# Performance work log

Measured on AMD Instinct MI355X. Metric: run time of the kernel, lower is better.

## Reference

```python
import jax, jax.numpy as jnp
import numpy as np

B, L, J, D_MODEL, N_HIDDEN = 8, 2048, 2048, 1024, 1024


def setup_inputs() -> dict:
    key = jax.random.key(0)
    ks = jax.random.split(key, 6)
    scale = 1.0 / np.sqrt(D_MODEL)
    return {
        "q": jax.random.normal(ks[0], (B, L, D_MODEL), dtype=jnp.float32),
        "k": jax.random.normal(ks[1], (B, J, D_MODEL), dtype=jnp.float32),
        "v": jax.random.normal(ks[2], (B, J, D_MODEL), dtype=jnp.float32),
        "mask": jnp.zeros((B, L, J), dtype=jnp.float32),
        # Linear(d_model, n_hidden, bias=False) weights, stored [n_hidden, d_model] like torch
        "W_q": jax.random.normal(ks[3], (N_HIDDEN, D_MODEL), dtype=jnp.float32) * scale,
        "W_k": jax.random.normal(ks[4], (N_HIDDEN, D_MODEL), dtype=jnp.float32) * scale,
        "W_v": jax.random.normal(ks[5], (N_HIDDEN, D_MODEL), dtype=jnp.float32) * scale,
    }


def reference(q, k, v, mask, W_q, W_k, W_v):
    # Linear projections (torch Linear: x @ W.T)
    qp = jnp.einsum('bld,hd->blh', q, W_q)
    kp = jnp.einsum('bjd,hd->bjh', k, W_k)
    vp = jnp.einsum('bjd,hd->bjh', v, W_v)
    # scaled dot-product scores [B, L, J]
    scores = jnp.einsum('blh,bjh->blj', qp, kp) / jnp.sqrt(jnp.float32(N_HIDDEN)).astype(qp.dtype)
    scores = scores + mask
    attn = jax.nn.softmax(scores, axis=-1)
    return jnp.einsum('blj,bjh->blh', attn, vp)
```

## Files before the change

kernel.cpp:

```cpp
#include <hip/hip_runtime.h>
#include <hip/hip_fp16.h>

typedef _Float16 f16;
typedef __attribute__((ext_vector_type(8))) _Float16 f16x8;
typedef __attribute__((ext_vector_type(4))) _Float16 f16x4;
typedef __attribute__((ext_vector_type(4))) float f32x4;

#define BM 128
#define BN 128
#define BK 64

__device__ __forceinline__ void gll16(const void* src, void* dst) {
  __builtin_amdgcn_global_load_lds((const __attribute__((address_space(1))) void*)src,
                                   (__attribute__((address_space(3))) void*)dst,
                                   16, 0, 0);
}

template<int MODE>
__global__ __launch_bounds__(256, 3)
void gemm_bt(const f16* __restrict__ Aall, const f16* __restrict__ Ball,
             void* __restrict__ Call,
             int M, int N, int K, int lda, int ldb, int ldc,
             long strideA, long strideB, long strideC,
             const float* __restrict__ maskAll, long strideMask,
             float* __restrict__ lvec, float scale)
{
  __shared__ __align__(16) f16 smA[BM * BK];
  __shared__ __align__(16) f16 smB[BN * BK];

  unsigned gx = gridDim.x, gy = gridDim.y;
  unsigned id = (blockIdx.z * gy + blockIdx.y) * gx + blockIdx.x;
  unsigned nwg = gx * gy * gridDim.z;
  unsigned swz = (id & 7) * (nwg >> 3) + (id >> 3);
  unsigned bx = swz % gx, rem = swz / gx;
  unsigned by = rem % gy, bz = rem / gy;

  const int z = bz;
  const f16* A = Aall + (long)z * strideA;
  const f16* B = Ball + (long)z * strideB;

  const int tid  = threadIdx.x;
  const int wid  = tid >> 6;
  const int lane = tid & 63;
  const int wm = wid >> 1;
  const int wn = wid & 1;
  const int lr = lane & 15;
  const int g  = lane >> 4;

  const long brow = (long)by * BM;
  const long bcol = (long)bx * BN;
  const int  nt   = K / BK;

  f32x4 acc[4][4] = {};

  auto stA = [&](int t) {
    #pragma unroll
    for (int i = 0; i < 4; ++i) {
      int c  = i * 256 + tid;
      int r  = c >> 3;
      int sl = (c & 7) ^ (r & 7);
      gll16(A + (brow + r) * (long)lda + t * BK + sl * 8, &smA[c * 8]);
    }
  };
  auto stB = [&](int t) {
    #pragma unroll
    for (int i = 0; i < 4; ++i) {
      int c  = i * 256 + tid;
      int r  = c >> 3;
      int sl = (c & 7) ^ (r & 7);
      gll16(B + (bcol + r) * (long)ldb + t * BK + sl * 8, &smB[c * 8]);
    }
  };

  for (int t = 0; t < nt; ++t) {
    stA(t); stB(t);
    __syncthreads();
    f16x8 af[8], bf[8];
    #pragma unroll
    for (int fm = 0; fm < 4; ++fm)
      #pragma unroll
      for (int ks = 0; ks < 2; ++ks) {
        int r = wm * 64 + fm * 16 + lr;
        af[fm * 2 + ks] = *(const f16x8*)(smA + r * BK + ((ks * 4 + g) ^ (r & 7)) * 8);
      }
    #pragma unroll
    for (int fn = 0; fn < 4; ++fn)
      #pragma unroll
      for (int ks = 0; ks < 2; ++ks) {
        int r = wn * 64 + fn * 16 + lr;
        bf[fn * 2 + ks] = *(const f16x8*)(smB + r * BK + ((ks * 4 + g) ^ (r & 7)) * 8);
      }
    #pragma unroll
    for (int fm = 0; fm < 4; ++fm)
      #pragma unroll
      for (int fn = 0; fn < 4; ++fn)
        #pragma unroll
        for (int ks = 0; ks < 2; ++ks)
          acc[fm][fn] = __builtin_amdgcn_mfma_f32_16x16x32_f16(
              af[fm * 2 + ks], bf[fn * 2 + ks], acc[fm][fn], 0, 0, 0);
    __syncthreads();
  }

  const int rb = (lane >> 4) * 4;

  if (MODE == 0) {
    f16* C = (f16*)Call + (long)z * strideC;
    #pragma unroll
    for (int m = 0; m < 4; ++m)
      #pragma unroll
      for (int j = 0; j < 4; ++j) {
        long grow = brow + wm * 64 + m * 16 + rb + j;
        #pragma unroll
        for (int n = 0; n < 4; ++n) {
          long gcol = bcol + wn * 64 + n * 16 + lr;
          C[grow * ldc + gcol] = (f16)acc[m][n][j];
        }
      }
  } else if (MODE == 1) {
    f16* C = (f16*)Call + (long)z * strideC;
    const float* mask = maskAll + (long)z * strideMask;
    #pragma unroll
    for (int m = 0; m < 4; ++m)
      #pragma unroll
      for (int j = 0; j < 4; ++j) {
        long grow = brow + wm * 64 + m * 16 + rb + j;
        float s = 0.f;
        #pragma unroll
        for (int n = 0; n < 4; ++n) {
          long gcol = bcol + wn * 64 + n * 16 + lr;
          float p = __expf(acc[m][n][j] * scale + mask[grow * ldc + gcol]);
          C[grow * ldc + gcol] = (f16)p;
          s += p;
        }
        s += __shfl_xor(s, 1);
        s += __shfl_xor(s, 2);
        s += __shfl_xor(s, 4);
        s += __shfl_xor(s, 8);
        if (lr == 0)
          lvec[((long)z * M + grow) * 32 + bx * 2 + wn] = s;
      }
  } else {
    float* C = (float*)Call + (long)z * strideC;
    #pragma unroll
    for (int m = 0; m < 4; ++m)
      #pragma unroll
      for (int j = 0; j < 4; ++j) {
        long grow = brow + wm * 64 + m * 16 + rb + j;
        float inv = 1.0f / lvec[(long)z * M + grow];
        #pragma unroll
        for (int n = 0; n < 4; ++n) {
          long gcol = bcol + wn * 64 + n * 16 + lr;
          C[grow * ldc + gcol] = acc[m][n][j] * inv;
        }
      }
  }
}

__global__ void cvt_all(const float* __restrict__ q, const float* __restrict__ k,
                        const float* __restrict__ v, const float* __restrict__ Wq,
                        const float* __restrict__ Wk, const float* __restrict__ Wv,
                        f16* __restrict__ qf, f16* __restrict__ kf, f16* __restrict__ vf,
                        f16* __restrict__ Wqf, f16* __restrict__ Wkf, f16* __restrict__ Wvf)
{
  const long NQ4 = 4194304, NW4 = 262144;
  const long total = 3 * NQ4 + 3 * NW4;
  for (long i = (long)blockIdx.x * blockDim.x + threadIdx.x; i < total;
       i += (long)gridDim.x * blockDim.x) {
    const float* src; f16* dst; long j = i;
    if      (j <     NQ4)           { src = q;  dst = qf; }
    else if (j < 2 * NQ4)           { src = k;  dst = kf;  j -= NQ4; }
    else if (j < 3 * NQ4)           { src = v;  dst = vf;  j -= 2 * NQ4; }
    else if (j < 3 * NQ4 + NW4)     { src = Wq; dst = Wqf; j -= 3 * NQ4; }
    else if (j < 3 * NQ4 + 2 * NW4) { src = Wk; dst = Wkf; j -= 3 * NQ4 + NW4; }
    else                            { src = Wv; dst = Wvf; j -= 3 * NQ4 + 2 * NW4; }
    float4 vv = ((const float4*)src)[j];
    f16x4 o;
    o[0] = (f16)vv.x; o[1] = (f16)vv.y; o[2] = (f16)vv.z; o[3] = (f16)vv.w;
    ((f16x4*)dst)[j] = o;
  }
}

__global__ void reduce_l(const float* __restrict__ lpart, float* __restrict__ lsum, int n) {
  int i = blockIdx.x * blockDim.x + threadIdx.x;
  if (i < n) {
    float s = 0.f;
    #pragma unroll
    for (int j = 0; j < 32; ++j) s += lpart[(long)i * 32 + j];
    lsum[i] = s;
  }
}

extern "C" void kernel_launch(void* const* d_in, const int* in_sizes, int n_in,
                              void* d_out, int out_size, void* d_ws, size_t ws_size,
                              hipStream_t stream)
{
  const float* q    = (const float*)d_in[0];
  const float* k    = (const float*)d_in[1];
  const float* v    = (const float*)d_in[2];
  const float* mask = (const float*)d_in[3];
  const float* Wq   = (const float*)d_in[4];
  const float* Wk   = (const float*)d_in[5];
  const float* Wv   = (const float*)d_in[6];
  float* out = (float*)d_out;
  char*  ws  = (char*)d_ws;

  f16* qf  = (f16*)(ws + 0);
  f16* kf  = (f16*)(ws + 33554432);
  f16* vf  = (f16*)(ws + 67108864);
  f16* Pm  = (f16*)(ws + 0);
  f16* Wqf = (f16*)(ws + 100663296);
  f16* Wkf = (f16*)(ws + 102760448);
  f16* Wvf = (f16*)(ws + 104857600);
  f16* qp  = (f16*)(ws + 106954752);
  f16* kp  = (f16*)(ws + 140509184);
  f16* vpT = (f16*)(ws + 174063616);
  float* lpart = (float*)(ws + 207618048);
  float* lsum  = (float*)(ws + 209715200);

  const long L = 2048, J = 2048, D = 1024, H = 1024;

  cvt_all<<<dim3(2048), dim3(256), 0, stream>>>(q, k, v, Wq, Wk, Wv, qf, kf, vf, Wqf, Wkf, Wvf);

  gemm_bt<0><<<dim3(1024 / BN, 16384 / BM, 1), dim3(256), 0, stream>>>(
      qf, Wqf, qp, 16384, 1024, 1024, 1024, 1024, 1024,
      0, 0, 0, nullptr, 0, nullptr, 0.f);
  gemm_bt<0><<<dim3(1024 / BN, 16384 / BM, 1), dim3(256), 0, stream>>>(
      kf, Wkf, kp, 16384, 1024, 1024, 1024, 1024, 1024,
      0, 0, 0, nullptr, 0, nullptr, 0.f);
  gemm_bt<0><<<dim3(2048 / BN, 1024 / BM, 8), dim3(256), 0, stream>>>(
      Wvf, vf, vpT, 1024, 2048, 1024, 1024, 1024, 2048,
      0, J * D, H * J, nullptr, 0, nullptr, 0.f);

  gemm_bt<1><<<dim3(2048 / BN, 2048 / BM, 8), dim3(256), 0, stream>>>(
      qp, kp, Pm, 2048, 2048, 1024, 1024, 1024, 2048,
      L * H, J * H, L * J, mask, L * J, lpart, 0.03125f);

  reduce_l<<<dim3(16384 / 256), dim3(256), 0, stream>>>(lpart, lsum, 16384);

  gemm_bt<2><<<dim3(1024 / BN, 2048 / BM, 8), dim3(256), 0, stream>>>(
      Pm, vpT, out, 2048, 1024, 2048, 2048, 2048, 1024,
      L * J, H * J, L * H, nullptr, 0, lsum, 0.f);
}
```

Measured before the change: 359.4 us.

## Fold Q and K projections into a single precomputed Wq^T Wk matrix

Scores are computed as q·(Wq^T Wk)·k^T: a small 1024x1024 product G = Wq^T Wk is formed once, q is multiplied by G, and the score GEMM then uses the raw fp16 k directly. This drops the separate 16384x1024x1024 key projection GEMM and replaces it with a much smaller weight-weight GEMM plus a transpose kernel for Wq and Wk. The fp16 rounding of the combined matrix G changes numerics slightly relative to projecting each side separately.

```diff
diff --git a/kernel.cpp b/kernel.cpp
--- a/kernel.cpp
+++ b/kernel.cpp
@@ -157,26 +157,53 @@
 }
 
 __global__ void cvt_all(const float* __restrict__ q, const float* __restrict__ k,
-                        const float* __restrict__ v, const float* __restrict__ Wq,
-                        const float* __restrict__ Wk, const float* __restrict__ Wv,
+                        const float* __restrict__ v, const float* __restrict__ Wv,
                         f16* __restrict__ qf, f16* __restrict__ kf, f16* __restrict__ vf,
-                        f16* __restrict__ Wqf, f16* __restrict__ Wkf, f16* __restrict__ Wvf)
+                        f16* __restrict__ Wvf)
 {
   const long NQ4 = 4194304, NW4 = 262144;
-  const long total = 3 * NQ4 + 3 * NW4;
+  const long total = 3 * NQ4 + NW4;
   for (long i = (long)blockIdx.x * blockDim.x + threadIdx.x; i < total;
        i += (long)gridDim.x * blockDim.x) {
     const float* src; f16* dst; long j = i;
-    if      (j <     NQ4)           { src = q;  dst = qf; }
-    else if (j < 2 * NQ4)           { src = k;  dst = kf;  j -= NQ4; }
-    else if (j < 3 * NQ4)           { src = v;  dst = vf;  j -= 2 * NQ4; }
-    else if (j < 3 * NQ4 + NW4)     { src = Wq; dst = Wqf; j -= 3 * NQ4; }
-    else if (j < 3 * NQ4 + 2 * NW4) { src = Wk; dst = Wkf; j -= 3 * NQ4 + NW4; }
-    else                            { src = Wv; dst = Wvf; j -= 3 * NQ4 + 2 * NW4; }
+    if      (j <     NQ4) { src = q;  dst = qf; }
+    else if (j < 2 * NQ4) { src = k;  dst = kf;  j -= NQ4; }
+    else if (j < 3 * NQ4) { src = v;  dst = vf;  j -= 2 * NQ4; }
+    else                  { src = Wv; dst = Wvf; j -= 3 * NQ4; }
     float4 vv = ((const float4*)src)[j];
     f16x4 o;
     o[0] = (f16)vv.x; o[1] = (f16)vv.y; o[2] = (f16)vv.z; o[3] = (f16)vv.w;
     ((f16x4*)dst)[j] = o;
+  }
+}
+
+__global__ void transW(const float* __restrict__ Wq, const float* __restrict__ Wk,
+                       f16* __restrict__ WqT, f16* __restrict__ WkT)
+{
+  __shared__ f16 t[64][65];
+  const float* W  = blockIdx.z ? Wk : Wq;
+  f16*         WT = blockIdx.z ? WkT : WqT;
+  const int h0 = blockIdx.y * 64, d0 = blockIdx.x * 64;
+  const int tx = threadIdx.x & 15, ty = threadIdx.x >> 4;
+  #pragma unroll
+  for (int p = 0; p < 4; ++p) {
+    int h = ty + p * 16;
+    float4 vv = *(const float4*)(W + (long)(h0 + h) * 1024 + d0 + tx * 4);
+    t[tx * 4 + 0][h] = (f16)vv.x;
+    t[tx * 4 + 1][h] = (f16)vv.y;
+    t[tx * 4 + 2][h] = (f16)vv.z;
+    t[tx * 4 + 3][h] = (f16)vv.w;
+  }
+  __syncthreads();
+  #pragma unroll
+  for (int p = 0; p < 4; ++p) {
+    int d = ty + p * 16;
+    f16x4 o;
+    o[0] = t[d][tx * 4 + 0];
+    o[1] = t[d][tx * 4 + 1];
+    o[2] = t[d][tx * 4 + 2];
+    o[3] = t[d][tx * 4 + 3];
+    *(f16x4*)(WT + (long)(d0 + d) * 1024 + h0 + tx * 4) = o;
   }
 }
 
@@ -204,36 +231,39 @@
   float* out = (float*)d_out;
   char*  ws  = (char*)d_ws;
 
-  f16* qf  = (f16*)(ws + 0);
-  f16* kf  = (f16*)(ws + 33554432);
-  f16* vf  = (f16*)(ws + 67108864);
-  f16* Pm  = (f16*)(ws + 0);
-  f16* Wqf = (f16*)(ws + 100663296);
-  f16* Wkf = (f16*)(ws + 102760448);
-  f16* Wvf = (f16*)(ws + 104857600);
-  f16* qp  = (f16*)(ws + 106954752);
-  f16* kp  = (f16*)(ws + 140509184);
-  f16* vpT = (f16*)(ws + 174063616);
-  float* lpart = (float*)(ws + 207618048);
-  float* lsum  = (float*)(ws + 209715200);
+  f16*   qf    = (f16*)(ws + 0);
+  f16*   vf    = (f16*)(ws + 33554432);
+  f16*   Pm    = (f16*)(ws + 0);
+  f16*   kf    = (f16*)(ws + 67108864);
+  f16*   Wvf   = (f16*)(ws + 100663296);
+  f16*   WqT   = (f16*)(ws + 102760448);
+  f16*   WkT   = (f16*)(ws + 104857600);
+  f16*   Gt    = (f16*)(ws + 106954752);
+  f16*   qg    = (f16*)(ws + 109051904);
+  f16*   vpT   = (f16*)(ws + 142606336);
+  float* lpart = (float*)(ws + 176160768);
+  float* lsum  = (float*)(ws + 178257920);
 
   const long L = 2048, J = 2048, D = 1024, H = 1024;
 
-  cvt_all<<<dim3(2048), dim3(256), 0, stream>>>(q, k, v, Wq, Wk, Wv, qf, kf, vf, Wqf, Wkf, Wvf);
+  cvt_all<<<dim3(2048), dim3(256), 0, stream>>>(q, k, v, Wv, qf, kf, vf, Wvf);
+  transW<<<dim3(16, 16, 2), dim3(256), 0, stream>>>(Wq, Wk, WqT, WkT);
+
+  gemm_bt<0><<<dim3(1024 / BN, 1024 / BM, 1), dim3(256), 0, stream>>>(
+      WkT, WqT, Gt, 1024, 1024, 1024, 1024, 1024, 1024,
+      0, 0, 0, nullptr, 0, nullptr, 0.f);
 
   gemm_bt<0><<<dim3(1024 / BN, 16384 / BM, 1), dim3(256), 0, stream>>>(
-      qf, Wqf, qp, 16384, 1024, 1024, 1024, 1024, 1024,
+      qf, Gt, qg, 16384, 1024, 1024, 1024, 1024, 1024,
       0, 0, 0, nullptr, 0, nullptr, 0.f);
-  gemm_bt<0><<<dim3(1024 / BN, 16384 / BM, 1), dim3(256), 0, stream>>>(
-      kf, Wkf, kp, 16384, 1024, 1024, 1024, 1024, 1024,
-      0, 0, 0, nullptr, 0, nullptr, 0.f);
+
   gemm_bt<0><<<dim3(2048 / BN, 1024 / BM, 8), dim3(256), 0, stream>>>(
       Wvf, vf, vpT, 1024, 2048, 1024, 1024, 1024, 2048,
       0, J * D, H * J, nullptr, 0, nullptr, 0.f);
 
   gemm_bt<1><<<dim3(2048 / BN, 2048 / BM, 8), dim3(256), 0, stream>>>(
-      qp, kp, Pm, 2048, 2048, 1024, 1024, 1024, 2048,
-      L * H, J * H, L * J, mask, L * J, lpart, 0.03125f);
+      qg, kf, Pm, 2048, 2048, 1024, 1024, 1024, 2048,
+      L * D, J * D, L * J, mask, L * J, lpart, 0.03125f);
 
   reduce_l<<<dim3(16384 / 256), dim3(256), 0, stream>>>(lpart, lsum, 16384);
 
```

New measurement: 337.4 us, median of 2. 1.07x faster.
